# Kernel optimization log

Measured on AMD Instinct MI355X. Metric: run time of the kernel, lower is better.

## Reference

```python
import jax, jax.numpy as jnp
import numpy as np

B = 512          # batch of visual features
VF_D = 4096      # visual feature dim (VGG fc7)
HID_D = 2048     # hidden dim
EMB_D = 300      # order-embedding / label-vector dim
N_LABELS = 2000  # number of GT label vectors


def setup_inputs() -> dict:
    key = jax.random.key(0)
    ks = jax.random.split(key, 4)
    vfs = jax.random.normal(ks[0], (B, VF_D), dtype=jnp.float32)
    W1 = jax.random.normal(ks[1], (VF_D, HID_D), dtype=jnp.float32) * (1.0 / np.sqrt(VF_D))
    b1 = jnp.zeros((HID_D,), dtype=jnp.float32)
    W2 = jax.random.normal(ks[2], (HID_D, EMB_D), dtype=jnp.float32) * (1.0 / np.sqrt(HID_D))
    b2 = jnp.zeros((EMB_D,), dtype=jnp.float32)
    gt_label_vecs = jax.random.normal(ks[3], (N_LABELS, EMB_D), dtype=jnp.float32)
    return {"vfs": vfs, "W1": W1, "b1": b1, "W2": W2, "b2": b2,
            "gt_label_vecs": gt_label_vecs}


def reference(vfs, W1, b1, W2, b2, gt_label_vecs):
    # hidden_layer: ReLU -> (Dropout, identity at eval) -> Linear
    vf_hidden = jnp.dot(jax.nn.relu(vfs), W1) + b1            # [B, HID_D]
    # embedding_layer: ReLU -> Linear
    vf_emb = jnp.dot(jax.nn.relu(vf_hidden), W2) + b2         # [B, EMB_D]
    # order_sim(hypers=gt_label_vecs, hypos=vf_emb):
    #   score = -|| clamp(hypo - hyper, min=0) ||^2, batched over all pairs
    diff = jax.nn.relu(vf_emb[:, None, :] - gt_label_vecs[None, :, :])  # [B, N, D]
    score_stack = -jnp.sum(diff * diff, axis=-1)              # [B, N_LABELS]
    return score_stack, vf_emb
```

## Files before the change

kernel.cpp:

```cpp
#include <hip/hip_runtime.h>

#define B_SZ   512
#define VFD    4096
#define HIDD   2048
#define EMBD   300
#define NLAB   2000
#define NPAD   320

#define G1_SPLIT 4
#define G2_SPLIT 8
#define SD_SPLIT 4

typedef __attribute__((ext_vector_type(8))) short short8x;
typedef __attribute__((ext_vector_type(4))) float f32x4;
typedef __attribute__((ext_vector_type(8))) unsigned short ushort8;
typedef __attribute__((ext_vector_type(4))) unsigned short ushort4x;

typedef const __attribute__((address_space(1))) unsigned int* gas_t;
typedef __attribute__((address_space(3))) unsigned int* las_t;

__device__ inline unsigned short f2bf(float x) {
    unsigned u = __float_as_uint(x);
    u += 0x7FFF + ((u >> 16) & 1);
    return (unsigned short)(u >> 16);
}

__global__ __launch_bounds__(256) void prep_kernel(
    const float* __restrict__ vfs, unsigned short* __restrict__ Xb,
    const float* __restrict__ W1, unsigned short* __restrict__ W1T,
    const float* __restrict__ W2, unsigned short* __restrict__ W2T,
    float* __restrict__ scores, const float* __restrict__ b2,
    float* __restrict__ E)
{
    __shared__ unsigned int Lds[64][34];
    const int tid = threadIdx.x;
    const int blk = blockIdx.x;

    if (blk < 1024) {
        const int i = (blk * 256 + tid) * 8;
        float4 a = *(const float4*)&vfs[i];
        float4 b = *(const float4*)&vfs[i + 4];
        ushort8 o;
        o[0] = f2bf(fmaxf(a.x, 0.f)); o[1] = f2bf(fmaxf(a.y, 0.f));
        o[2] = f2bf(fmaxf(a.z, 0.f)); o[3] = f2bf(fmaxf(a.w, 0.f));
        o[4] = f2bf(fmaxf(b.x, 0.f)); o[5] = f2bf(fmaxf(b.y, 0.f));
        o[6] = f2bf(fmaxf(b.z, 0.f)); o[7] = f2bf(fmaxf(b.w, 0.f));
        *(ushort8*)&Xb[i] = o;
        return;
    }
    if (blk >= 4232) {
        const int j = ((blk - 4232) * 256 + tid) * 4;
        if (j < B_SZ * EMBD) {
            const int n = j % EMBD;
            *(float4*)&E[j] = *(const float4*)&b2[n];
        }
        return;
    }
    if (blk >= 3232) {
        const int i = ((blk - 3232) * 256 + tid) * 4;
        if (i < B_SZ * NLAB) {
            float4 z = {0.f, 0.f, 0.f, 0.f};
            *(float4*)&scores[i] = z;
        }
        return;
    }

    const float* in; unsigned short* out; int N, ldK, bx, by;
    if (blk < 3072) {
        const int b = blk - 1024;
        in = W1; out = W1T; N = HIDD; ldK = VFD; bx = b & 31; by = b >> 5;
    } else {
        const int b = blk - 3072;
        in = W2; out = W2T; N = EMBD; ldK = HIDD; bx = b % 5; by = b / 5;
    }
    const int n0 = bx * 64, k0 = by * 64;

    #pragma unroll
    for (int i = 0; i < 2; ++i) {
        const int s = tid + 256 * i;
        const int kp = s >> 4, nq = s & 15;
        const int n = n0 + nq * 4;
        float4 v0 = {0.f,0.f,0.f,0.f}, v1 = {0.f,0.f,0.f,0.f};
        if (n < N) {
            v0 = *(const float4*)&in[(size_t)(k0 + 2 * kp)     * N + n];
            v1 = *(const float4*)&in[(size_t)(k0 + 2 * kp + 1) * N + n];
        }
        Lds[nq*4+0][kp] = (unsigned)f2bf(v0.x) | ((unsigned)f2bf(v1.x) << 16);
        Lds[nq*4+1][kp] = (unsigned)f2bf(v0.y) | ((unsigned)f2bf(v1.y) << 16);
        Lds[nq*4+2][kp] = (unsigned)f2bf(v0.z) | ((unsigned)f2bf(v1.z) << 16);
        Lds[nq*4+3][kp] = (unsigned)f2bf(v0.w) | ((unsigned)f2bf(v1.w) << 16);
    }
    __syncthreads();

    #pragma unroll
    for (int i = 0; i < 2; ++i) {
        const int c = tid + 256 * i;
        const int n = c >> 3, oct = c & 7;
        uint2 lo = *(uint2*)&Lds[n][oct * 4];
        uint2 hi = *(uint2*)&Lds[n][oct * 4 + 2];
        uint4 v = make_uint4(lo.x, lo.y, hi.x, hi.y);
        *(uint4*)&out[(size_t)(n0 + n) * ldK + k0 + oct * 8] = v;
    }
}

__global__ __launch_bounds__(256) void gemm1_kernel(
    const unsigned short* __restrict__ A,
    const unsigned short* __restrict__ Bt,
    float* __restrict__ Cpart)
{
    __shared__ unsigned short As[2][4096];
    __shared__ unsigned short Bs[2][8192];

    const int tid = threadIdx.x;
    const int m0 = blockIdx.y * 64, n0 = blockIdx.x * 128;
    const int kbase = blockIdx.z * (VFD / G1_SPLIT);

    const unsigned short* ga = A + (size_t)(m0 + (tid & 63)) * VFD + kbase + (tid >> 6) * 8;
    const unsigned short* gb = Bt + (size_t)(n0 + (tid & 127)) * VFD + kbase + (tid >> 7) * 8;

    const int lane = tid & 63;
    const int wave = tid >> 6;
    const int wm = (wave & 1) * 32;
    const int wn = (wave >> 1) * 64;
    const int q = lane >> 4, l15 = lane & 15;

    f32x4 acc[2][4];
    #pragma unroll
    for (int r = 0; r < 2; ++r)
        #pragma unroll
        for (int c = 0; c < 4; ++c) acc[r][c] = (f32x4){0.f,0.f,0.f,0.f};

    #pragma unroll
    for (int i = 0; i < 2; ++i)
        __builtin_amdgcn_global_load_lds((gas_t)(const void*)(ga + i * 32),
                                         (las_t)(void*)&As[0][(tid + 256 * i) * 8], 16, 0, 0);
    #pragma unroll
    for (int i = 0; i < 4; ++i)
        __builtin_amdgcn_global_load_lds((gas_t)(const void*)(gb + i * 16),
                                         (las_t)(void*)&Bs[0][(tid + 256 * i) * 8], 16, 0, 0);

    const int iters = (VFD / G1_SPLIT) / 64;
    for (int t = 0; t < iters; ++t) {
        const int cur = t & 1, nxt = cur ^ 1;
        __syncthreads();

        if (t + 1 < iters) {
            const int ko = (t + 1) * 64;
            #pragma unroll
            for (int i = 0; i < 2; ++i)
                __builtin_amdgcn_global_load_lds((gas_t)(const void*)(ga + ko + i * 32),
                                                 (las_t)(void*)&As[nxt][(tid + 256 * i) * 8], 16, 0, 0);
            #pragma unroll
            for (int i = 0; i < 4; ++i)
                __builtin_amdgcn_global_load_lds((gas_t)(const void*)(gb + ko + i * 16),
                                                 (las_t)(void*)&Bs[nxt][(tid + 256 * i) * 8], 16, 0, 0);
        }

        #pragma unroll
        for (int kk = 0; kk < 2; ++kk) {
            const int oct = kk * 4 + q;
            short8x a0 = *(short8x*)&As[cur][(oct * 64 + wm +      l15) * 8];
            short8x a1 = *(short8x*)&As[cur][(oct * 64 + wm + 16 + l15) * 8];
            #pragma unroll
            for (int c = 0; c < 4; ++c) {
                short8x b = *(short8x*)&Bs[cur][(oct * 128 + wn + c * 16 + l15) * 8];
                acc[0][c] = __builtin_amdgcn_mfma_f32_16x16x32_bf16(a0, b, acc[0][c], 0, 0, 0);
                acc[1][c] = __builtin_amdgcn_mfma_f32_16x16x32_bf16(a1, b, acc[1][c], 0, 0, 0);
            }
        }
    }

    float* Cz = Cpart + (size_t)blockIdx.z * B_SZ * HIDD;
    #pragma unroll
    for (int r = 0; r < 2; ++r)
        #pragma unroll
        for (int g = 0; g < 4; ++g) {
            const int rr = m0 + wm + r * 16 + q * 4 + g;
            #pragma unroll
            for (int c = 0; c < 4; ++c)
                Cz[(size_t)rr * HIDD + n0 + wn + c * 16 + l15] = acc[r][c][g];
        }
}

__global__ __launch_bounds__(256) void reduce_h_kernel(
    const float* __restrict__ Hpart, const float* __restrict__ b1,
    unsigned short* __restrict__ Hb)
{
    const int i = (blockIdx.x * 256 + threadIdx.x) * 4;
    const int col = i & (HIDD - 1);
    float4 s = *(const float4*)&b1[col];
    #pragma unroll
    for (int z = 0; z < G1_SPLIT; ++z) {
        float4 p = *(const float4*)&Hpart[(size_t)z * B_SZ * HIDD + i];
        s.x += p.x; s.y += p.y; s.z += p.z; s.w += p.w;
    }
    ushort4x o;
    o[0] = f2bf(fmaxf(s.x, 0.f));
    o[1] = f2bf(fmaxf(s.y, 0.f));
    o[2] = f2bf(fmaxf(s.z, 0.f));
    o[3] = f2bf(fmaxf(s.w, 0.f));
    *(ushort4x*)&Hb[i] = o;
}

__global__ __launch_bounds__(256) void gemm2_kernel(
    const unsigned short* __restrict__ A,
    const unsigned short* __restrict__ Bt,
    float* __restrict__ E)
{
    __shared__ unsigned short As[2][4096];
    __shared__ unsigned short Bs[2][4096];

    const int tid = threadIdx.x;
    const int m0 = blockIdx.y * 64, n0 = blockIdx.x * 64;
    const int kbase = blockIdx.z * (HIDD / G2_SPLIT);

    const unsigned short* ga = A  + (size_t)(m0 + (tid & 63)) * HIDD + kbase + (tid >> 6) * 8;
    const unsigned short* gb = Bt + (size_t)(n0 + (tid & 63)) * HIDD + kbase + (tid >> 6) * 8;

    const int lane = tid & 63;
    const int wave = tid >> 6;
    const int wm = (wave & 1) * 32;
    const int wn = (wave >> 1) * 32;
    const int q = lane >> 4, l15 = lane & 15;

    f32x4 acc00 = {0.f,0.f,0.f,0.f}, acc01 = {0.f,0.f,0.f,0.f};
    f32x4 acc10 = {0.f,0.f,0.f,0.f}, acc11 = {0.f,0.f,0.f,0.f};

    #pragma unroll
    for (int i = 0; i < 2; ++i) {
        __builtin_amdgcn_global_load_lds((gas_t)(const void*)(ga + i * 32),
                                         (las_t)(void*)&As[0][(tid + 256 * i) * 8], 16, 0, 0);
        __builtin_amdgcn_global_load_lds((gas_t)(const void*)(gb + i * 32),
                                         (las_t)(void*)&Bs[0][(tid + 256 * i) * 8], 16, 0, 0);
    }

    const int iters = (HIDD / G2_SPLIT) / 64;
    for (int t = 0; t < iters; ++t) {
        const int cur = t & 1, nxt = cur ^ 1;
        __syncthreads();

        if (t + 1 < iters) {
            const int ko = (t + 1) * 64;
            #pragma unroll
            for (int i = 0; i < 2; ++i) {
                __builtin_amdgcn_global_load_lds((gas_t)(const void*)(ga + ko + i * 32),
                                                 (las_t)(void*)&As[nxt][(tid + 256 * i) * 8], 16, 0, 0);
                __builtin_amdgcn_global_load_lds((gas_t)(const void*)(gb + ko + i * 32),
                                                 (las_t)(void*)&Bs[nxt][(tid + 256 * i) * 8], 16, 0, 0);
            }
        }

        #pragma unroll
        for (int kk = 0; kk < 2; ++kk) {
            const int oct = kk * 4 + q;
            short8x a0 = *(short8x*)&As[cur][(oct * 64 + wm +      l15) * 8];
            short8x a1 = *(short8x*)&As[cur][(oct * 64 + wm + 16 + l15) * 8];
            short8x b0 = *(short8x*)&Bs[cur][(oct * 64 + wn +      l15) * 8];
            short8x b1 = *(short8x*)&Bs[cur][(oct * 64 + wn + 16 + l15) * 8];
            acc00 = __builtin_amdgcn_mfma_f32_16x16x32_bf16(a0, b0, acc00, 0, 0, 0);
            acc01 = __builtin_amdgcn_mfma_f32_16x16x32_bf16(a0, b1, acc01, 0, 0, 0);
            acc10 = __builtin_amdgcn_mfma_f32_16x16x32_bf16(a1, b0, acc10, 0, 0, 0);
            acc11 = __builtin_amdgcn_mfma_f32_16x16x32_bf16(a1, b1, acc11, 0, 0, 0);
        }
    }

    const int cc = n0 + wn + l15;
    #pragma unroll
    for (int r = 0; r < 4; ++r) {
        const int rr = m0 + wm + q * 4 + r;
        if (cc < EMBD)      atomicAdd(&E[(size_t)rr * EMBD + cc],        acc00[r]);
        if (cc + 16 < EMBD) atomicAdd(&E[(size_t)rr * EMBD + cc + 16],   acc01[r]);
        if (cc < EMBD)      atomicAdd(&E[(size_t)(rr + 16) * EMBD + cc], acc10[r]);
        if (cc + 16 < EMBD) atomicAdd(&E[(size_t)(rr + 16) * EMBD + cc + 16], acc11[r]);
    }
}

__global__ __launch_bounds__(128) void scores_part_kernel(
    const float* __restrict__ E, const float* __restrict__ G,
    float* __restrict__ scores)
{
    __shared__ float Gs[64][44];

    const int tid = threadIdx.x;
    const int tx = tid & 15, ty = tid >> 4;
    const int n0 = blockIdx.x * 64, b0 = blockIdx.y * 32;
    const int dbase = blockIdx.z * (NPAD / SD_SPLIT);

    float acc[4][4] = {};

    for (int dc = 0; dc < NPAD / SD_SPLIT; dc += 40) {
        const int d0 = dbase + dc;
        __syncthreads();
        #pragma unroll
        for (int i = 0; i < 5; ++i) {
            const int s = tid + 128 * i;
            const int row = s / 10, qd = (s - row * 10) * 4;
            const int d = d0 + qd;
            const int n = n0 + row;
            float4 v = {0.f, 0.f, 0.f, 0.f};
            if (n < NLAB && d < EMBD) v = *(const float4*)&G[(size_t)n * EMBD + d];
            *(float4*)&Gs[row][qd] = v;
        }
        __syncthreads();

        #pragma unroll 2
        for (int d = 0; d < 40; d += 4) {
            const int dd = d0 + d;
            float4 e[4];
            if (dd < EMBD) {
                #pragma unroll
                for (int r = 0; r < 4; ++r)
                    e[r] = *(const float4*)&E[(size_t)(b0 + ty * 4 + r) * EMBD + dd];
            } else {
                #pragma unroll
                for (int r = 0; r < 4; ++r) e[r] = make_float4(0.f, 0.f, 0.f, 0.f);
            }
            #pragma unroll
            for (int c = 0; c < 4; ++c) {
                float4 g = *(float4*)&Gs[tx + 16 * c][d];
                #pragma unroll
                for (int r = 0; r < 4; ++r) {
                    float t;
                    t = fmaxf(e[r].x - g.x, 0.f); acc[r][c] += t * t;
                    t = fmaxf(e[r].y - g.y, 0.f); acc[r][c] += t * t;
                    t = fmaxf(e[r].z - g.z, 0.f); acc[r][c] += t * t;
                    t = fmaxf(e[r].w - g.w, 0.f); acc[r][c] += t * t;
                }
            }
        }
    }

    #pragma unroll
    for (int r = 0; r < 4; ++r) {
        const int b = b0 + ty * 4 + r;
        #pragma unroll
        for (int c = 0; c < 4; ++c) {
            const int n = n0 + tx + 16 * c;
            if (n < NLAB) atomicAdd(&scores[(size_t)b * NLAB + n], -acc[r][c]);
        }
    }
}

extern "C" void kernel_launch(void* const* d_in, const int* in_sizes, int n_in,
                              void* d_out, int out_size, void* d_ws, size_t ws_size,
                              hipStream_t stream)
{
    const float* vfs = (const float*)d_in[0];
    const float* W1  = (const float*)d_in[1];
    const float* b1  = (const float*)d_in[2];
    const float* W2  = (const float*)d_in[3];
    const float* b2  = (const float*)d_in[4];
    const float* G   = (const float*)d_in[5];

    float* out    = (float*)d_out;
    float* scores = out;
    float* E      = out + (size_t)B_SZ * NLAB;

    char* ws = (char*)d_ws;
    unsigned short* Xb  = (unsigned short*)(ws);
    unsigned short* W1T = (unsigned short*)(ws + 4194304);
    unsigned short* W2T = (unsigned short*)(ws + 20971520);
    unsigned short* Hb  = (unsigned short*)(ws + 22282240);
    float*          Hpart = (float*)(ws + 24379392);

    prep_kernel<<<4382, 256, 0, stream>>>(vfs, Xb, W1, W1T, W2, W2T,
                                          scores, b2, E);

    gemm1_kernel<<<dim3(16, 8, G1_SPLIT), 256, 0, stream>>>(Xb, W1T, Hpart);
    reduce_h_kernel<<<1024, 256, 0, stream>>>(Hpart, b1, Hb);

    gemm2_kernel<<<dim3(5, 8, G2_SPLIT), 256, 0, stream>>>(Hb, W2T, E);

    scores_part_kernel<<<dim3(32, 16, SD_SPLIT), 128, 0, stream>>>(E, G, scores);
}
```

Measured before the change: 171.7 us.

## Fuse split-K reduction into atomics and ReLU/bf16 conversion into GEMM2 load

The separate reduce_h kernel goes away. gemm1 now atomically accumulates its split-K partials into an fp32 hidden buffer, which the prep kernel pre-initialises with b1. gemm2 reads that fp32 buffer directly and applies ReLU and the bf16 pack in registers before writing to LDS, which costs one A-tile buffer plus an extra barrier. Separately, the scores kernel doubles its per-thread batch rows (8 instead of 4) and halves its grid, increasing register reuse of G tiles. The cost is float atomic contention on H, gemm2 reading fp32 (twice the bytes), and higher register pressure in the scores kernel.

```diff
diff --git a/kernel.cpp b/kernel.cpp
--- a/kernel.cpp
+++ b/kernel.cpp
@@ -14,7 +14,6 @@
 typedef __attribute__((ext_vector_type(8))) short short8x;
 typedef __attribute__((ext_vector_type(4))) float f32x4;
 typedef __attribute__((ext_vector_type(8))) unsigned short ushort8;
-typedef __attribute__((ext_vector_type(4))) unsigned short ushort4x;
 
 typedef const __attribute__((address_space(1))) unsigned int* gas_t;
 typedef __attribute__((address_space(3))) unsigned int* las_t;
@@ -23,6 +22,9 @@
     unsigned u = __float_as_uint(x);
     u += 0x7FFF + ((u >> 16) & 1);
     return (unsigned short)(u >> 16);
+}
+__device__ inline unsigned pack2relu(float a, float b) {
+    return (unsigned)f2bf(fmaxf(a, 0.f)) | ((unsigned)f2bf(fmaxf(b, 0.f)) << 16);
 }
 
 __global__ __launch_bounds__(256) void prep_kernel(
@@ -30,7 +32,8 @@
     const float* __restrict__ W1, unsigned short* __restrict__ W1T,
     const float* __restrict__ W2, unsigned short* __restrict__ W2T,
     float* __restrict__ scores, const float* __restrict__ b2,
-    float* __restrict__ E)
+    float* __restrict__ E, const float* __restrict__ b1,
+    float* __restrict__ H)
 {
     __shared__ unsigned int Lds[64][34];
     const int tid = threadIdx.x;
@@ -48,6 +51,12 @@
         *(ushort8*)&Xb[i] = o;
         return;
     }
+    if (blk >= 4382) {
+        const int i = ((blk - 4382) * 256 + tid) * 4;
+        const int col = i & (HIDD - 1);
+        *(float4*)&H[i] = *(const float4*)&b1[col];
+        return;
+    }
     if (blk >= 4232) {
         const int j = ((blk - 4232) * 256 + tid) * 4;
         if (j < B_SZ * EMBD) {
@@ -106,7 +115,7 @@
 __global__ __launch_bounds__(256) void gemm1_kernel(
     const unsigned short* __restrict__ A,
     const unsigned short* __restrict__ Bt,
-    float* __restrict__ Cpart)
+    float* __restrict__ H)
 {
     __shared__ unsigned short As[2][4096];
     __shared__ unsigned short Bs[2][8192];
@@ -170,7 +179,6 @@
         }
     }
 
-    float* Cz = Cpart + (size_t)blockIdx.z * B_SZ * HIDD;
     #pragma unroll
     for (int r = 0; r < 2; ++r)
         #pragma unroll
@@ -178,43 +186,23 @@
             const int rr = m0 + wm + r * 16 + q * 4 + g;
             #pragma unroll
             for (int c = 0; c < 4; ++c)
-                Cz[(size_t)rr * HIDD + n0 + wn + c * 16 + l15] = acc[r][c][g];
-        }
-}
-
-__global__ __launch_bounds__(256) void reduce_h_kernel(
-    const float* __restrict__ Hpart, const float* __restrict__ b1,
-    unsigned short* __restrict__ Hb)
-{
-    const int i = (blockIdx.x * 256 + threadIdx.x) * 4;
-    const int col = i & (HIDD - 1);
-    float4 s = *(const float4*)&b1[col];
-    #pragma unroll
-    for (int z = 0; z < G1_SPLIT; ++z) {
-        float4 p = *(const float4*)&Hpart[(size_t)z * B_SZ * HIDD + i];
-        s.x += p.x; s.y += p.y; s.z += p.z; s.w += p.w;
-    }
-    ushort4x o;
-    o[0] = f2bf(fmaxf(s.x, 0.f));
-    o[1] = f2bf(fmaxf(s.y, 0.f));
-    o[2] = f2bf(fmaxf(s.z, 0.f));
-    o[3] = f2bf(fmaxf(s.w, 0.f));
-    *(ushort4x*)&Hb[i] = o;
+                atomicAdd(&H[(size_t)rr * HIDD + n0 + wn + c * 16 + l15], acc[r][c][g]);
+        }
 }
 
 __global__ __launch_bounds__(256) void gemm2_kernel(
-    const unsigned short* __restrict__ A,
+    const float* __restrict__ H,
     const unsigned short* __restrict__ Bt,
     float* __restrict__ E)
 {
-    __shared__ unsigned short As[2][4096];
+    __shared__ unsigned short As[4096];
     __shared__ unsigned short Bs[2][4096];
 
     const int tid = threadIdx.x;
     const int m0 = blockIdx.y * 64, n0 = blockIdx.x * 64;
     const int kbase = blockIdx.z * (HIDD / G2_SPLIT);
 
-    const unsigned short* ga = A  + (size_t)(m0 + (tid & 63)) * HIDD + kbase + (tid >> 6) * 8;
+    const float* gha = H + (size_t)(m0 + (tid & 63)) * HIDD + kbase + (tid >> 6) * 8;
     const unsigned short* gb = Bt + (size_t)(n0 + (tid & 63)) * HIDD + kbase + (tid >> 6) * 8;
 
     const int lane = tid & 63;
@@ -226,35 +214,47 @@
     f32x4 acc00 = {0.f,0.f,0.f,0.f}, acc01 = {0.f,0.f,0.f,0.f};
     f32x4 acc10 = {0.f,0.f,0.f,0.f}, acc11 = {0.f,0.f,0.f,0.f};
 
-    #pragma unroll
-    for (int i = 0; i < 2; ++i) {
-        __builtin_amdgcn_global_load_lds((gas_t)(const void*)(ga + i * 32),
-                                         (las_t)(void*)&As[0][(tid + 256 * i) * 8], 16, 0, 0);
+    float4 p00 = *(const float4*)(gha);
+    float4 p01 = *(const float4*)(gha + 4);
+    float4 p10 = *(const float4*)(gha + 32);
+    float4 p11 = *(const float4*)(gha + 36);
+    #pragma unroll
+    for (int i = 0; i < 2; ++i)
         __builtin_amdgcn_global_load_lds((gas_t)(const void*)(gb + i * 32),
                                          (las_t)(void*)&Bs[0][(tid + 256 * i) * 8], 16, 0, 0);
-    }
 
     const int iters = (HIDD / G2_SPLIT) / 64;
     for (int t = 0; t < iters; ++t) {
         const int cur = t & 1, nxt = cur ^ 1;
+
+        {
+            uint4 u0, u1;
+            u0.x = pack2relu(p00.x, p00.y); u0.y = pack2relu(p00.z, p00.w);
+            u0.z = pack2relu(p01.x, p01.y); u0.w = pack2relu(p01.z, p01.w);
+            u1.x = pack2relu(p10.x, p10.y); u1.y = pack2relu(p10.z, p10.w);
+            u1.z = pack2relu(p11.x, p11.y); u1.w = pack2relu(p11.z, p11.w);
+            *(uint4*)&As[tid * 8]         = u0;
+            *(uint4*)&As[(tid + 256) * 8] = u1;
+        }
         __syncthreads();
 
         if (t + 1 < iters) {
             const int ko = (t + 1) * 64;
             #pragma unroll
-            for (int i = 0; i < 2; ++i) {
-                __builtin_amdgcn_global_load_lds((gas_t)(const void*)(ga + ko + i * 32),
-                                                 (las_t)(void*)&As[nxt][(tid + 256 * i) * 8], 16, 0, 0);
+            for (int i = 0; i < 2; ++i)
                 __builtin_amdgcn_global_load_lds((gas_t)(const void*)(gb + ko + i * 32),
                                                  (las_t)(void*)&Bs[nxt][(tid + 256 * i) * 8], 16, 0, 0);
-            }
+            p00 = *(const float4*)(gha + ko);
+            p01 = *(const float4*)(gha + ko + 4);
+            p10 = *(const float4*)(gha + ko + 32);
+            p11 = *(const float4*)(gha + ko + 36);
         }
 
         #pragma unroll
         for (int kk = 0; kk < 2; ++kk) {
             const int oct = kk * 4 + q;
-            short8x a0 = *(short8x*)&As[cur][(oct * 64 + wm +      l15) * 8];
-            short8x a1 = *(short8x*)&As[cur][(oct * 64 + wm + 16 + l15) * 8];
+            short8x a0 = *(short8x*)&As[(oct * 64 + wm +      l15) * 8];
+            short8x a1 = *(short8x*)&As[(oct * 64 + wm + 16 + l15) * 8];
             short8x b0 = *(short8x*)&Bs[cur][(oct * 64 + wn +      l15) * 8];
             short8x b1 = *(short8x*)&Bs[cur][(oct * 64 + wn + 16 + l15) * 8];
             acc00 = __builtin_amdgcn_mfma_f32_16x16x32_bf16(a0, b0, acc00, 0, 0, 0);
@@ -262,6 +262,7 @@
             acc10 = __builtin_amdgcn_mfma_f32_16x16x32_bf16(a1, b0, acc10, 0, 0, 0);
             acc11 = __builtin_amdgcn_mfma_f32_16x16x32_bf16(a1, b1, acc11, 0, 0, 0);
         }
+        __syncthreads();
     }
 
     const int cc = n0 + wn + l15;
@@ -283,10 +284,10 @@
 
     const int tid = threadIdx.x;
     const int tx = tid & 15, ty = tid >> 4;
-    const int n0 = blockIdx.x * 64, b0 = blockIdx.y * 32;
+    const int n0 = blockIdx.x * 64, b0 = blockIdx.y * 64;
     const int dbase = blockIdx.z * (NPAD / SD_SPLIT);
 
-    float acc[4][4] = {};
+    float acc[8][4] = {};
 
     for (int dc = 0; dc < NPAD / SD_SPLIT; dc += 40) {
         const int d0 = dbase + dc;
@@ -303,23 +304,22 @@
         }
         __syncthreads();
 
-        #pragma unroll 2
         for (int d = 0; d < 40; d += 4) {
             const int dd = d0 + d;
-            float4 e[4];
+            float4 e[8];
             if (dd < EMBD) {
                 #pragma unroll
-                for (int r = 0; r < 4; ++r)
-                    e[r] = *(const float4*)&E[(size_t)(b0 + ty * 4 + r) * EMBD + dd];
+                for (int r = 0; r < 8; ++r)
+                    e[r] = *(const float4*)&E[(size_t)(b0 + ty * 8 + r) * EMBD + dd];
             } else {
                 #pragma unroll
-                for (int r = 0; r < 4; ++r) e[r] = make_float4(0.f, 0.f, 0.f, 0.f);
+                for (int r = 0; r < 8; ++r) e[r] = make_float4(0.f, 0.f, 0.f, 0.f);
             }
             #pragma unroll
             for (int c = 0; c < 4; ++c) {
                 float4 g = *(float4*)&Gs[tx + 16 * c][d];
                 #pragma unroll
-                for (int r = 0; r < 4; ++r) {
+                for (int r = 0; r < 8; ++r) {
                     float t;
                     t = fmaxf(e[r].x - g.x, 0.f); acc[r][c] += t * t;
                     t = fmaxf(e[r].y - g.y, 0.f); acc[r][c] += t * t;
@@ -331,8 +331,8 @@
     }
 
     #pragma unroll
-    for (int r = 0; r < 4; ++r) {
-        const int b = b0 + ty * 4 + r;
+    for (int r = 0; r < 8; ++r) {
+        const int b = b0 + ty * 8 + r;
         #pragma unroll
         for (int c = 0; c < 4; ++c) {
             const int n = n0 + tx + 16 * c;
@@ -360,16 +360,14 @@
     unsigned short* Xb  = (unsigned short*)(ws);
     unsigned short* W1T = (unsigned short*)(ws + 4194304);
     unsigned short* W2T = (unsigned short*)(ws + 20971520);
-    unsigned short* Hb  = (unsigned short*)(ws + 22282240);
-    float*          Hpart = (float*)(ws + 24379392);
-
-    prep_kernel<<<4382, 256, 0, stream>>>(vfs, Xb, W1, W1T, W2, W2T,
-                                          scores, b2, E);
-
-    gemm1_kernel<<<dim3(16, 8, G1_SPLIT), 256, 0, stream>>>(Xb, W1T, Hpart);
-    reduce_h_kernel<<<1024, 256, 0, stream>>>(Hpart, b1, Hb);
-
-    gemm2_kernel<<<dim3(5, 8, G2_SPLIT), 256, 0, stream>>>(Hb, W2T, E);
-
-    scores_part_kernel<<<dim3(32, 16, SD_SPLIT), 128, 0, stream>>>(E, G, scores);
-}
+    float*          H   = (float*)(ws + 22282240);
+
+    prep_kernel<<<5406, 256, 0, stream>>>(vfs, Xb, W1, W1T, W2, W2T,
+                                          scores, b2, E, b1, H);
+
+    gemm1_kernel<<<dim3(16, 8, G1_SPLIT), 256, 0, stream>>>(Xb, W1T, H);
+
+    gemm2_kernel<<<dim3(5, 8, G2_SPLIT), 256, 0, stream>>>(H, W2T, E);
+
+    scores_part_kernel<<<dim3(32, 8, SD_SPLIT), 128, 0, stream>>>(E, G, scores);
+}
```

Measured after the change: 190.5 us. 1.11x slower.
